# Optimization experiments

Hardware: AMD Instinct MI355X
Metric: run time of the kernel (lower is better)

Reference implementation:

```python
import jax, jax.numpy as jnp
import numpy as np

B, C, CI, HM, HC = 4, 64, 32, 128, 64  # batch, in_channels, inter_channels, main HW, cross HW
BN_EPS = 1e-5


def conv1x1(x, w, b):
    # x: [B,Cin,H,W], w: [Cout,Cin], b: [Cout]
    return jnp.einsum('bchw,oc->bohw', x, w) + b[None, :, None, None]


def _lin_coords(n_in, n_out):
    # PyTorch bilinear, align_corners=False: src = (i+0.5)*scale - 0.5, clamped
    scale = n_in / n_out
    src = (jnp.arange(n_out, dtype=jnp.float32) + 0.5) * scale - 0.5
    src = jnp.clip(src, 0.0, n_in - 1)
    i0 = jnp.floor(src).astype(jnp.int32)
    i1 = jnp.minimum(i0 + 1, n_in - 1)
    w = src - i0.astype(jnp.float32)
    return i0, i1, w


def resize_bilinear(x, h_out, w_out):
    # x: [B,C,H,W] -> [B,C,h_out,w_out], matches torch F.interpolate(mode='bilinear', align_corners=False)
    _, _, h_in, w_in = x.shape
    i0, i1, wh = _lin_coords(h_in, h_out)
    x = x[:, :, i0, :] * (1.0 - wh)[None, None, :, None] + x[:, :, i1, :] * wh[None, None, :, None]
    j0, j1, ww = _lin_coords(w_in, w_out)
    x = x[:, :, :, j0] * (1.0 - ww)[None, None, None, :] + x[:, :, :, j1] * ww[None, None, None, :]
    return x


def setup_inputs() -> dict:
    key = jax.random.key(0)
    ks = jax.random.split(key, 12)
    p = lambda k, shape, s=0.05: jax.random.normal(k, shape, dtype=jnp.float32) * s
    return {
        'main_feature': jax.random.normal(ks[0], (B, C, HM, HM), dtype=jnp.float32),
        'cross_feature': jax.random.normal(ks[1], (B, C, HC, HC), dtype=jnp.float32),
        'g_w': p(ks[2], (CI, C)), 'g_b': p(ks[3], (CI,)),
        'theta_w': p(ks[4], (CI, C)), 'theta_b': p(ks[5], (CI,)),
        'phi_w': p(ks[6], (CI, C)), 'phi_b': p(ks[7], (CI,)),
        'w_w': p(ks[8], (C, CI)), 'w_b': p(ks[9], (C,)),
        'bn_gamma': 1.0 + p(ks[10], (C,)), 'bn_beta': p(ks[11], (C,)),
    }


def reference(main_feature, cross_feature, g_w, g_b, theta_w, theta_b,
              phi_w, phi_b, w_w, w_b, bn_gamma, bn_beta):
    b, _, hc, wc = cross_feature.shape
    hm = main_feature.shape[2]
    # g(cross) -> [B, Nc, Ci]
    x = conv1x1(cross_feature, g_w, g_b).reshape(b, CI, -1).transpose(0, 2, 1)
    # theta(cross) -> [B, Ci, Nc]
    y = conv1x1(cross_feature, theta_w, theta_b).reshape(b, CI, -1)
    # phi(resize(main -> cross size)) -> [B, Nc, Ci]
    z = resize_bilinear(main_feature, hc, hc)
    z = conv1x1(z, phi_w, phi_b).reshape(b, CI, -1).transpose(0, 2, 1)
    # unscaled attention: [B, Nc, Nc]
    f = jnp.einsum('bnc,bcm->bnm', x, y)
    attn = jax.nn.softmax(f, axis=-1)
    out = jnp.einsum('bnm,bmc->bnc', attn, z)           # [B, Nc, Ci]
    out = out.transpose(0, 2, 1).reshape(b, CI, hc, wc)  # [B, Ci, Hc, Wc]
    # W: 1x1 conv + BatchNorm2d (training mode: batch statistics, biased var)
    out = conv1x1(out, w_w, w_b)
    mean = out.mean(axis=(0, 2, 3), keepdims=True)
    var = out.var(axis=(0, 2, 3), keepdims=True)
    out = (out - mean) * jax.lax.rsqrt(var + BN_EPS)
    out = out * bn_gamma[None, :, None, None] + bn_beta[None, :, None, None]
    out = resize_bilinear(out, hm, hm)
    return out + main_feature
```

## Files before the change

### kernel.cpp

```cpp
#include <hip/hip_runtime.h>
#include <hip/hip_bf16.h>


typedef __attribute__((ext_vector_type(8))) short bf16x8;
typedef __attribute__((ext_vector_type(4))) float f32x4;

#define LOG2E 1.4426950408889634f

static __device__ __forceinline__ unsigned short f2bf_bits(float x) {
    __hip_bfloat16 h = __float2bfloat16(x);
    return *(unsigned short*)&h;
}
static __device__ __forceinline__ unsigned int pk2bf(float a, float b) {
    __hip_bfloat162 h = __float22bfloat162_rn(make_float2(a, b));
    return *(unsigned int*)&h;
}

__global__ __launch_bounds__(256) void qkv_kernel(
    const float* __restrict__ cross, const float* __restrict__ mainf,
    const float* __restrict__ g_w,  const float* __restrict__ g_b,
    const float* __restrict__ th_w, const float* __restrict__ th_b,
    const float* __restrict__ ph_w, const float* __restrict__ ph_b,
    __hip_bfloat16* __restrict__ Qb, __hip_bfloat16* __restrict__ Kb,
    __hip_bfloat16* __restrict__ Vt)
{
    __shared__ float xs[64][256];
    const int kind = blockIdx.x >> 6;
    const int pblk = blockIdx.x & 63;
    const int b = pblk >> 4, n0 = (pblk & 15) << 8;
    const int t = threadIdx.x;

    const float* w  = (kind == 0) ? g_w : (kind == 1) ? th_w : ph_w;
    const float* bs = (kind == 0) ? g_b : (kind == 1) ? th_b : ph_b;

    if (kind < 2) {
        const float* src = cross + (((size_t)(b * 64)) << 12) + n0;
        const int jr = (t & 63) << 2, c0 = t >> 6;
#pragma unroll
        for (int it = 0; it < 16; ++it) {
            int c = (it << 2) | c0;
            *(float4*)&xs[c][jr] = *(const float4*)(src + ((size_t)c << 12) + jr);
        }
    } else {
        const int n = n0 + t;
        const int i2 = (n >> 6) << 1, j2 = (n & 63) << 1;
        const float* src = mainf + (((size_t)(b * 64)) << 14) + i2 * 128 + j2;
#pragma unroll 4
        for (int c = 0; c < 64; ++c) {
            const float2 a = *(const float2*)(src + ((size_t)c << 14));
            const float2 d = *(const float2*)(src + ((size_t)c << 14) + 128);
            xs[c][t] = 0.25f * ((a.x + a.y) + (d.x + d.y));
        }
    }
    __syncthreads();

    float acc[32];
#pragma unroll
    for (int ci = 0; ci < 32; ++ci) acc[ci] = bs[ci];
#pragma unroll 4
    for (int c = 0; c < 64; ++c) {
        float x = xs[c][t];
#pragma unroll
        for (int ci = 0; ci < 32; ++ci)
            acc[ci] = fmaf(w[(ci << 6) + c], x, acc[ci]);
    }

    const int pix = (b << 12) + n0 + t;
    if (kind < 2) {
        if (kind == 0) {
#pragma unroll
            for (int ci = 0; ci < 32; ++ci) acc[ci] *= LOG2E;
        }
        unsigned int u[16];
#pragma unroll
        for (int i = 0; i < 16; ++i)
            u[i] = (unsigned int)f2bf_bits(acc[2 * i]) |
                   ((unsigned int)f2bf_bits(acc[2 * i + 1]) << 16);
        __hip_bfloat16* dst = ((kind == 0) ? Qb : Kb) + (size_t)pix * 32;
        uint4* d4 = (uint4*)dst;
#pragma unroll
        for (int r = 0; r < 4; ++r)
            d4[r] = make_uint4(u[4*r], u[4*r+1], u[4*r+2], u[4*r+3]);
    } else {
        const int n = n0 + t;
#pragma unroll
        for (int ci = 0; ci < 32; ++ci)
            Vt[((size_t)((b << 5) | ci) << 12) + n] = __float2bfloat16(acc[ci]);
    }
}

__global__ __launch_bounds__(256) void attn_mfma(
    const __hip_bfloat16* __restrict__ Qb, const __hip_bfloat16* __restrict__ Kb,
    const __hip_bfloat16* __restrict__ Vt, const float* __restrict__ w_w,
    const float* __restrict__ w_b, float* __restrict__ out2)
{
    __shared__ __align__(16) __hip_bfloat16 pbuf[4][2][16][40];
    __shared__ __align__(16) float redbuf[2][64][12];
    __shared__ __align__(16) float obuf[32][36];
    const int tid = threadIdx.x, lane = tid & 63, w = tid >> 6;
    const int lo = lane & 15, c = lane >> 4;
    const int kh = w & 1, qg = w >> 1;
    const int b = blockIdx.y;
    const int qbase = (blockIdx.x << 5) + (qg << 4);

    const bf16x8 aq = *(const bf16x8*)(Qb + (((size_t)(b << 12) + qbase + lo) << 5) + (c << 3));
    const __hip_bfloat16* Kbb = Kb + ((size_t)(b << 12) << 5);
    const __hip_bfloat16* Vbb = Vt + ((size_t)(b << 5) << 12);

    f32x4 acc0 = {0.f,0.f,0.f,0.f}, acc1 = {0.f,0.f,0.f,0.f};
    float den = 0.f;
    const f32x4 z = {0.f,0.f,0.f,0.f};
    const int kq = kh << 11;
#define LDK(k)      (*(const bf16x8*)(Kbb + ((size_t)((k) + lo) << 5) + (c << 3)))
#define LDV(k, cio) (*(const bf16x8*)(Vbb + ((size_t)(lo + (cio)) << 12) + (k) + (c << 3)))

    bf16x8 k0c = LDK(kq),      k1c = LDK(kq + 16);
    bf16x8 vB0 = LDV(kq, 0),   vB1 = LDV(kq, 16);
    bf16x8 k0n = LDK(kq + 32), k1n = LDK(kq + 48);
    bf16x8 vN0 = LDV(kq + 32, 0), vN1 = LDV(kq + 32, 16);
    bf16x8 ap;

    {
        f32x4 s0 = __builtin_amdgcn_mfma_f32_16x16x32_bf16(k0c, aq, z, 0, 0, 0);
        f32x4 s1 = __builtin_amdgcn_mfma_f32_16x16x32_bf16(k1c, aq, z, 0, 0, 0);
        float p0 = __builtin_amdgcn_exp2f(s0[0]), p1 = __builtin_amdgcn_exp2f(s0[1]);
        float p2 = __builtin_amdgcn_exp2f(s0[2]), p3 = __builtin_amdgcn_exp2f(s0[3]);
        float q0 = __builtin_amdgcn_exp2f(s1[0]), q1 = __builtin_amdgcn_exp2f(s1[1]);
        float q2 = __builtin_amdgcn_exp2f(s1[2]), q3 = __builtin_amdgcn_exp2f(s1[3]);
        den += ((p0 + p1) + (p2 + p3)) + ((q0 + q1) + (q2 + q3));
        uint2 wv0 = make_uint2(pk2bf(p0, p1), pk2bf(p2, p3));
        uint2 wv1 = make_uint2(pk2bf(q0, q1), pk2bf(q2, q3));
        *(uint2*)&pbuf[w][0][lo][c << 2]        = wv0;
        *(uint2*)&pbuf[w][0][lo][16 + (c << 2)] = wv1;
        ap = *(const bf16x8*)&pbuf[w][0][lo][c << 3];
    }

#pragma unroll 2
    for (int ch = 1; ch < 64; ++ch) {
        const int kn = kq + ((ch + 1) & 63) * 32;
        bf16x8 vA0 = vB0, vA1 = vB1;
        vB0 = vN0; vB1 = vN1;
        k0c = k0n; k1c = k1n;
        k0n = LDK(kn); k1n = LDK(kn + 16);
        vN0 = LDV(kn, 0); vN1 = LDV(kn, 16);

        f32x4 s0 = __builtin_amdgcn_mfma_f32_16x16x32_bf16(k0c, aq, z, 0, 0, 0);
        f32x4 s1 = __builtin_amdgcn_mfma_f32_16x16x32_bf16(k1c, aq, z, 0, 0, 0);
        float p0 = __builtin_amdgcn_exp2f(s0[0]), p1 = __builtin_amdgcn_exp2f(s0[1]);
        float p2 = __builtin_amdgcn_exp2f(s0[2]), p3 = __builtin_amdgcn_exp2f(s0[3]);
        float q0 = __builtin_amdgcn_exp2f(s1[0]), q1 = __builtin_amdgcn_exp2f(s1[1]);
        float q2 = __builtin_amdgcn_exp2f(s1[2]), q3 = __builtin_amdgcn_exp2f(s1[3]);
        den += ((p0 + p1) + (p2 + p3)) + ((q0 + q1) + (q2 + q3));
        uint2 wv0 = make_uint2(pk2bf(p0, p1), pk2bf(p2, p3));
        uint2 wv1 = make_uint2(pk2bf(q0, q1), pk2bf(q2, q3));
        *(uint2*)&pbuf[w][ch & 1][lo][c << 2]        = wv0;
        *(uint2*)&pbuf[w][ch & 1][lo][16 + (c << 2)] = wv1;

        acc0 = __builtin_amdgcn_mfma_f32_16x16x32_bf16(ap, vA0, acc0, 0, 0, 0);
        acc1 = __builtin_amdgcn_mfma_f32_16x16x32_bf16(ap, vA1, acc1, 0, 0, 0);

        ap = *(const bf16x8*)&pbuf[w][ch & 1][lo][c << 3];
    }
    acc0 = __builtin_amdgcn_mfma_f32_16x16x32_bf16(ap, vB0, acc0, 0, 0, 0);
    acc1 = __builtin_amdgcn_mfma_f32_16x16x32_bf16(ap, vB1, acc1, 0, 0, 0);
#undef LDK
#undef LDV

    den += __shfl_xor(den, 16);
    den += __shfl_xor(den, 32);

    if (kh) {
        f32x4* rb = (f32x4*)&redbuf[qg][lane][0];
        rb[0] = acc0; rb[1] = acc1;
        f32x4 dv = {den, 0.f, 0.f, 0.f};
        rb[2] = dv;
    }
    __syncthreads();
    if (kh == 0) {
        const f32x4* rb = (const f32x4*)&redbuf[qg][lane][0];
        f32x4 a0 = rb[0], a1 = rb[1], dv = rb[2];
        acc0 += a0; acc1 += a1;
        den += dv[0];
#pragma unroll
        for (int r = 0; r < 4; ++r) {
            float inv = 1.0f / __shfl(den, (c << 2) | r);
            obuf[(qg << 4) | (c << 2) | r][lo]      = acc0[r] * inv;
            obuf[(qg << 4) | (c << 2) | r][16 + lo] = acc1[r] * inv;
        }
    }
    __syncthreads();

    const int q = tid & 31, cog = tid >> 5;
    float ov[32];
    const float4* orow = (const float4*)&obuf[q][0];
#pragma unroll
    for (int k4 = 0; k4 < 8; ++k4) {
        float4 t = orow[k4];
        ov[4*k4] = t.x; ov[4*k4+1] = t.y; ov[4*k4+2] = t.z; ov[4*k4+3] = t.w;
    }
    float* dstbase = out2 + (((size_t)(b << 6)) << 12) + (blockIdx.x << 5) + q;
#pragma unroll
    for (int kk = 0; kk < 8; ++kk) {
        int co = (kk << 3) | cog;
        const float4* wr = (const float4*)&w_w[co << 5];
        float acc = w_b[co];
#pragma unroll
        for (int k4 = 0; k4 < 8; ++k4) {
            float4 t = wr[k4];
            acc = fmaf(t.x, ov[4*k4],   acc);
            acc = fmaf(t.y, ov[4*k4+1], acc);
            acc = fmaf(t.z, ov[4*k4+2], acc);
            acc = fmaf(t.w, ov[4*k4+3], acc);
        }
        dstbase[(size_t)co << 12] = acc;
    }
}

__global__ __launch_bounds__(256) void stats_kernel(
    const float* __restrict__ out2, float* __restrict__ stats1)
{
    int co = blockIdx.x >> 2, b = blockIdx.x & 3, t = threadIdx.x;
    const float* p = out2 + ((size_t)((b << 6) | co) << 12);
    float s = 0.f, s2 = 0.f;
#pragma unroll
    for (int ii = 0; ii < 16; ++ii) {
        float v = p[(ii << 8) | t];
        s += v; s2 = fmaf(v, v, s2);
    }
    __shared__ float rs[256], rs2[256];
    rs[t] = s; rs2[t] = s2;
    __syncthreads();
    for (int off = 128; off > 0; off >>= 1) {
        if (t < off) { rs[t] += rs[t + off]; rs2[t] += rs2[t + off]; }
        __syncthreads();
    }
    if (t == 0) {
        stats1[blockIdx.x * 2]     = rs[0];
        stats1[blockIdx.x * 2 + 1] = rs2[0];
    }
}

__global__ __launch_bounds__(256) void up_kernel(
    const float* __restrict__ out2, const float* __restrict__ stats1,
    const float* __restrict__ gamma, const float* __restrict__ beta,
    const float* __restrict__ mainf, float* __restrict__ out)
{
    int gid = blockIdx.x * 256 + threadIdx.x;
    int j4 = (gid & 31) << 2;
    int i  = (gid >> 5) & 127;
    int co = (gid >> 12) & 63;
    int b  = gid >> 18;

    float sm = 0.f, sq = 0.f;
#pragma unroll
    for (int bb = 0; bb < 4; ++bb) {
        sm += stats1[((co << 2) | bb) * 2];
        sq += stats1[((co << 2) | bb) * 2 + 1];
    }
    float mean = sm * (1.0f / 16384.0f);
    float var  = sq * (1.0f / 16384.0f) - mean * mean;
    float inv  = rsqrtf(var + 1e-5f);
    float scale = gamma[co] * inv;
    float shift = beta[co] - mean * scale;

    int ih = i >> 1;
    int k0, k1; float wi;
    if (i & 1)       { k0 = ih;     k1 = (ih < 63) ? ih + 1 : 63; wi = 0.25f; }
    else if (ih == 0){ k0 = 0;      k1 = 0;                       wi = 0.0f;  }
    else             { k0 = ih - 1; k1 = ih;                      wi = 0.75f; }

    const float* p0r = out2 + ((size_t)((b << 6) | co) << 12) + (k0 << 6);
    const float* p1r = out2 + ((size_t)((b << 6) | co) << 12) + (k1 << 6);

    float res[4];
#pragma unroll
    for (int jj = 0; jj < 4; ++jj) {
        int j = j4 | jj;
        int il = j >> 1;
        int l0, l1; float wj;
        if (j & 1)       { l0 = il;     l1 = (il < 63) ? il + 1 : 63; wj = 0.25f; }
        else if (il == 0){ l0 = 0;      l1 = 0;                       wj = 0.0f;  }
        else             { l0 = il - 1; l1 = il;                      wj = 0.75f; }
        float v00 = p0r[l0], v01 = p0r[l1];
        float v10 = p1r[l0], v11 = p1r[l1];
        float top = v00 + wj * (v01 - v00);
        float bot = v10 + wj * (v11 - v10);
        float v = top + wi * (bot - top);
        res[jj] = fmaf(v, scale, shift);
    }
    size_t idx = (((size_t)((b << 6) | co)) << 14) + (i << 7) + j4;
    float4 m4 = *(const float4*)(mainf + idx);
    *(float4*)(out + idx) = make_float4(res[0] + m4.x, res[1] + m4.y,
                                        res[2] + m4.z, res[3] + m4.w);
}

extern "C" void kernel_launch(void* const* d_in, const int* in_sizes, int n_in,
                              void* d_out, int out_size, void* d_ws, size_t ws_size,
                              hipStream_t stream)
{
    const float* mainf = (const float*)d_in[0];
    const float* cross = (const float*)d_in[1];
    const float* g_w   = (const float*)d_in[2];
    const float* g_b   = (const float*)d_in[3];
    const float* th_w  = (const float*)d_in[4];
    const float* th_b  = (const float*)d_in[5];
    const float* ph_w  = (const float*)d_in[6];
    const float* ph_b  = (const float*)d_in[7];
    const float* w_w   = (const float*)d_in[8];
    const float* w_b   = (const float*)d_in[9];
    const float* gamma = (const float*)d_in[10];
    const float* beta  = (const float*)d_in[11];
    float* out = (float*)d_out;

    __hip_bfloat16* Qb = (__hip_bfloat16*)d_ws;
    __hip_bfloat16* Kb = Qb + 524288;
    __hip_bfloat16* Vt = Kb + 524288;
    float* out2   = (float*)(Vt + 524288);
    float* stats1 = out2 + 1048576;

    qkv_kernel<<<192, 256, 0, stream>>>(cross, mainf, g_w, g_b, th_w, th_b,
                                        ph_w, ph_b, Qb, Kb, Vt);
    attn_mfma<<<dim3(128, 4), 256, 0, stream>>>(Qb, Kb, Vt, w_w, w_b, out2);
    stats_kernel<<<256, 256, 0, stream>>>(out2, stats1);
    up_kernel<<<4096, 256, 0, stream>>>(out2, stats1, gamma, beta, mainf, out);
}
```

Before: 170.5 us.

## Fuse all stages into one persistent kernel with grid barriers

Merges the QKV projection, attention, BN statistics and upsample kernels into a single 512-block kernel separated by two software grid barriers. BN statistics are now accumulated with atomics in the attention epilogue, which removes the separate stats pass. The QKV stage is re-split into 384 smaller blocks so it spreads over more CUs. This removes per-launch overhead and one full read of out2. It relies on all 512 blocks being co-resident, which launch_bounds(256,2) is meant to ensure, and adds an init kernel plus barrier spin cost.

```diff
diff --git a/kernel.cpp b/kernel.cpp
--- a/kernel.cpp
+++ b/kernel.cpp
@@ -16,282 +16,303 @@
     return *(unsigned int*)&h;
 }
 
-__global__ __launch_bounds__(256) void qkv_kernel(
-    const float* __restrict__ cross, const float* __restrict__ mainf,
+union __align__(16) Smem {
+    float xs[64][128];
+    struct {
+        __hip_bfloat16 pbuf[4][2][16][40];
+        float redbuf[2][64][12];
+        float obuf[32][36];
+    } at;
+};
+
+__global__ __launch_bounds__(256) void init_kernel(float* stats, unsigned* bar) {
+    if (threadIdx.x < 128) stats[threadIdx.x] = 0.f;
+    if (threadIdx.x < 2)   bar[threadIdx.x] = 0u;
+}
+
+static __device__ __forceinline__ void grid_barrier(unsigned* bar, int idx) {
+    __threadfence();
+    __syncthreads();
+    if (threadIdx.x == 0) {
+        atomicAdd(&bar[idx], 1u);
+        while (__hip_atomic_load(&bar[idx], __ATOMIC_RELAXED,
+                                 __HIP_MEMORY_SCOPE_AGENT) < 512u) {
+            __builtin_amdgcn_s_sleep(2);
+        }
+    }
+    __syncthreads();
+    __threadfence();
+}
+
+__global__ __launch_bounds__(256, 2) void mega_kernel(
+    const float* __restrict__ mainf, const float* __restrict__ cross,
     const float* __restrict__ g_w,  const float* __restrict__ g_b,
     const float* __restrict__ th_w, const float* __restrict__ th_b,
     const float* __restrict__ ph_w, const float* __restrict__ ph_b,
+    const float* __restrict__ w_w,  const float* __restrict__ w_b,
+    const float* __restrict__ gamma, const float* __restrict__ beta,
     __hip_bfloat16* __restrict__ Qb, __hip_bfloat16* __restrict__ Kb,
-    __hip_bfloat16* __restrict__ Vt)
+    __hip_bfloat16* __restrict__ Vt, float* __restrict__ out2,
+    float* __restrict__ stats, unsigned* __restrict__ bar,
+    float* __restrict__ out)
 {
-    __shared__ float xs[64][256];
-    const int kind = blockIdx.x >> 6;
-    const int pblk = blockIdx.x & 63;
-    const int b = pblk >> 4, n0 = (pblk & 15) << 8;
-    const int t = threadIdx.x;
-
-    const float* w  = (kind == 0) ? g_w : (kind == 1) ? th_w : ph_w;
-    const float* bs = (kind == 0) ? g_b : (kind == 1) ? th_b : ph_b;
-
-    if (kind < 2) {
-        const float* src = cross + (((size_t)(b * 64)) << 12) + n0;
-        const int jr = (t & 63) << 2, c0 = t >> 6;
-#pragma unroll
-        for (int it = 0; it < 16; ++it) {
-            int c = (it << 2) | c0;
-            *(float4*)&xs[c][jr] = *(const float4*)(src + ((size_t)c << 12) + jr);
-        }
-    } else {
-        const int n = n0 + t;
-        const int i2 = (n >> 6) << 1, j2 = (n & 63) << 1;
-        const float* src = mainf + (((size_t)(b * 64)) << 14) + i2 * 128 + j2;
+    __shared__ Smem smem;
+    const int tid = threadIdx.x;
+
+    {
+        const int kb = blockIdx.x;
+        if (kb < 384) {
+            const int kind = kb >> 7;
+            const int sub  = kb & 127;
+            const int b    = sub >> 5;
+            const int n0   = (sub & 31) << 7;
+            const float* w  = (kind == 0) ? g_w : (kind == 1) ? th_w : ph_w;
+            const float* bs = (kind == 0) ? g_b : (kind == 1) ? th_b : ph_b;
+
+            if (kind < 2) {
+                const float* src = cross + (((size_t)(b * 64)) << 12) + n0;
+                const int jr = (tid & 31) << 2, c0 = tid >> 5;
+#pragma unroll
+                for (int it = 0; it < 8; ++it) {
+                    int c = (it << 3) | c0;
+                    *(float4*)&smem.xs[c][jr] = *(const float4*)(src + ((size_t)c << 12) + jr);
+                }
+            } else {
+                const int px = tid & 127, chh = tid >> 7;
+                const int n = n0 + px;
+                const int i2 = (n >> 6) << 1, j2 = (n & 63) << 1;
+                const float* src = mainf + (((size_t)(b * 64)) << 14) + i2 * 128 + j2;
 #pragma unroll 4
-        for (int c = 0; c < 64; ++c) {
-            const float2 a = *(const float2*)(src + ((size_t)c << 14));
-            const float2 d = *(const float2*)(src + ((size_t)c << 14) + 128);
-            xs[c][t] = 0.25f * ((a.x + a.y) + (d.x + d.y));
+                for (int cc = 0; cc < 32; ++cc) {
+                    int c = (chh << 5) | cc;
+                    const float2 a = *(const float2*)(src + ((size_t)c << 14));
+                    const float2 d = *(const float2*)(src + ((size_t)c << 14) + 128);
+                    smem.xs[c][px] = 0.25f * ((a.x + a.y) + (d.x + d.y));
+                }
+            }
+            __syncthreads();
+
+            const int px = tid & 127, cih = tid >> 7, ci0 = cih << 4;
+            float acc[16];
+#pragma unroll
+            for (int j = 0; j < 16; ++j) acc[j] = bs[ci0 + j];
+#pragma unroll 4
+            for (int c = 0; c < 64; ++c) {
+                float x = smem.xs[c][px];
+#pragma unroll
+                for (int j = 0; j < 16; ++j)
+                    acc[j] = fmaf(w[((ci0 + j) << 6) + c], x, acc[j]);
+            }
+            const int n = n0 + px;
+            const int pix = (b << 12) + n;
+            if (kind < 2) {
+                if (kind == 0) {
+#pragma unroll
+                    for (int j = 0; j < 16; ++j) acc[j] *= LOG2E;
+                }
+                unsigned int u[8];
+#pragma unroll
+                for (int i = 0; i < 8; ++i)
+                    u[i] = (unsigned int)f2bf_bits(acc[2 * i]) |
+                           ((unsigned int)f2bf_bits(acc[2 * i + 1]) << 16);
+                uint4* d4 = (uint4*)(((kind == 0) ? Qb : Kb) + (size_t)pix * 32 + ci0);
+                d4[0] = make_uint4(u[0], u[1], u[2], u[3]);
+                d4[1] = make_uint4(u[4], u[5], u[6], u[7]);
+            } else {
+#pragma unroll
+                for (int j = 0; j < 16; ++j)
+                    Vt[((size_t)((b << 5) | (ci0 + j)) << 12) + n] = __float2bfloat16(acc[j]);
+            }
         }
     }
-    __syncthreads();
-
-    float acc[32];
-#pragma unroll
-    for (int ci = 0; ci < 32; ++ci) acc[ci] = bs[ci];
-#pragma unroll 4
-    for (int c = 0; c < 64; ++c) {
-        float x = xs[c][t];
-#pragma unroll
-        for (int ci = 0; ci < 32; ++ci)
-            acc[ci] = fmaf(w[(ci << 6) + c], x, acc[ci]);
-    }
-
-    const int pix = (b << 12) + n0 + t;
-    if (kind < 2) {
-        if (kind == 0) {
-#pragma unroll
-            for (int ci = 0; ci < 32; ++ci) acc[ci] *= LOG2E;
-        }
-        unsigned int u[16];
-#pragma unroll
-        for (int i = 0; i < 16; ++i)
-            u[i] = (unsigned int)f2bf_bits(acc[2 * i]) |
-                   ((unsigned int)f2bf_bits(acc[2 * i + 1]) << 16);
-        __hip_bfloat16* dst = ((kind == 0) ? Qb : Kb) + (size_t)pix * 32;
-        uint4* d4 = (uint4*)dst;
-#pragma unroll
-        for (int r = 0; r < 4; ++r)
-            d4[r] = make_uint4(u[4*r], u[4*r+1], u[4*r+2], u[4*r+3]);
-    } else {
-        const int n = n0 + t;
-#pragma unroll
-        for (int ci = 0; ci < 32; ++ci)
-            Vt[((size_t)((b << 5) | ci) << 12) + n] = __float2bfloat16(acc[ci]);
-    }
-}
-
-__global__ __launch_bounds__(256) void attn_mfma(
-    const __hip_bfloat16* __restrict__ Qb, const __hip_bfloat16* __restrict__ Kb,
-    const __hip_bfloat16* __restrict__ Vt, const float* __restrict__ w_w,
-    const float* __restrict__ w_b, float* __restrict__ out2)
-{
-    __shared__ __align__(16) __hip_bfloat16 pbuf[4][2][16][40];
-    __shared__ __align__(16) float redbuf[2][64][12];
-    __shared__ __align__(16) float obuf[32][36];
-    const int tid = threadIdx.x, lane = tid & 63, w = tid >> 6;
-    const int lo = lane & 15, c = lane >> 4;
-    const int kh = w & 1, qg = w >> 1;
-    const int b = blockIdx.y;
-    const int qbase = (blockIdx.x << 5) + (qg << 4);
-
-    const bf16x8 aq = *(const bf16x8*)(Qb + (((size_t)(b << 12) + qbase + lo) << 5) + (c << 3));
-    const __hip_bfloat16* Kbb = Kb + ((size_t)(b << 12) << 5);
-    const __hip_bfloat16* Vbb = Vt + ((size_t)(b << 5) << 12);
-
-    f32x4 acc0 = {0.f,0.f,0.f,0.f}, acc1 = {0.f,0.f,0.f,0.f};
-    float den = 0.f;
-    const f32x4 z = {0.f,0.f,0.f,0.f};
-    const int kq = kh << 11;
+    grid_barrier(bar, 0);
+
+    {
+        const int lane = tid & 63, w = tid >> 6;
+        const int lo = lane & 15, c = lane >> 4;
+        const int kh = w & 1, qg = w >> 1;
+        const int b = blockIdx.x >> 7, bx = blockIdx.x & 127;
+        const int qbase = (bx << 5) + (qg << 4);
+
+        const bf16x8 aq = *(const bf16x8*)(Qb + (((size_t)(b << 12) + qbase + lo) << 5) + (c << 3));
+        const __hip_bfloat16* Kbb = Kb + ((size_t)(b << 12) << 5);
+        const __hip_bfloat16* Vbb = Vt + ((size_t)(b << 5) << 12);
+
+        f32x4 acc0 = {0.f,0.f,0.f,0.f}, acc1 = {0.f,0.f,0.f,0.f};
+        float den = 0.f;
+        const f32x4 z = {0.f,0.f,0.f,0.f};
+        const int kq = kh << 11;
 #define LDK(k)      (*(const bf16x8*)(Kbb + ((size_t)((k) + lo) << 5) + (c << 3)))
 #define LDV(k, cio) (*(const bf16x8*)(Vbb + ((size_t)(lo + (cio)) << 12) + (k) + (c << 3)))
 
-    bf16x8 k0c = LDK(kq),      k1c = LDK(kq + 16);
-    bf16x8 vB0 = LDV(kq, 0),   vB1 = LDV(kq, 16);
-    bf16x8 k0n = LDK(kq + 32), k1n = LDK(kq + 48);
-    bf16x8 vN0 = LDV(kq + 32, 0), vN1 = LDV(kq + 32, 16);
-    bf16x8 ap;
-
-    {
-        f32x4 s0 = __builtin_amdgcn_mfma_f32_16x16x32_bf16(k0c, aq, z, 0, 0, 0);
-        f32x4 s1 = __builtin_amdgcn_mfma_f32_16x16x32_bf16(k1c, aq, z, 0, 0, 0);
-        float p0 = __builtin_amdgcn_exp2f(s0[0]), p1 = __builtin_amdgcn_exp2f(s0[1]);
-        float p2 = __builtin_amdgcn_exp2f(s0[2]), p3 = __builtin_amdgcn_exp2f(s0[3]);
-        float q0 = __builtin_amdgcn_exp2f(s1[0]), q1 = __builtin_amdgcn_exp2f(s1[1]);
-        float q2 = __builtin_amdgcn_exp2f(s1[2]), q3 = __builtin_amdgcn_exp2f(s1[3]);
-        den += ((p0 + p1) + (p2 + p3)) + ((q0 + q1) + (q2 + q3));
-        uint2 wv0 = make_uint2(pk2bf(p0, p1), pk2bf(p2, p3));
-        uint2 wv1 = make_uint2(pk2bf(q0, q1), pk2bf(q2, q3));
-        *(uint2*)&pbuf[w][0][lo][c << 2]        = wv0;
-        *(uint2*)&pbuf[w][0][lo][16 + (c << 2)] = wv1;
-        ap = *(const bf16x8*)&pbuf[w][0][lo][c << 3];
-    }
+        bf16x8 k0c = LDK(kq),      k1c = LDK(kq + 16);
+        bf16x8 vB0 = LDV(kq, 0),   vB1 = LDV(kq, 16);
+        bf16x8 k0n = LDK(kq + 32), k1n = LDK(kq + 48);
+        bf16x8 vN0 = LDV(kq + 32, 0), vN1 = LDV(kq + 32, 16);
+        bf16x8 ap;
+
+        {
+            f32x4 s0 = __builtin_amdgcn_mfma_f32_16x16x32_bf16(k0c, aq, z, 0, 0, 0);
+            f32x4 s1 = __builtin_amdgcn_mfma_f32_16x16x32_bf16(k1c, aq, z, 0, 0, 0);
+            float p0 = __builtin_amdgcn_exp2f(s0[0]), p1 = __builtin_amdgcn_exp2f(s0[1]);
+            float p2 = __builtin_amdgcn_exp2f(s0[2]), p3 = __builtin_amdgcn_exp2f(s0[3]);
+            float q0 = __builtin_amdgcn_exp2f(s1[0]), q1 = __builtin_amdgcn_exp2f(s1[1]);
+            float q2 = __builtin_amdgcn_exp2f(s1[2]), q3 = __builtin_amdgcn_exp2f(s1[3]);
+            den += ((p0 + p1) + (p2 + p3)) + ((q0 + q1) + (q2 + q3));
+            uint2 wv0 = make_uint2(pk2bf(p0, p1), pk2bf(p2, p3));
+            uint2 wv1 = make_uint2(pk2bf(q0, q1), pk2bf(q2, q3));
+            *(uint2*)&smem.at.pbuf[w][0][lo][c << 2]        = wv0;
+            *(uint2*)&smem.at.pbuf[w][0][lo][16 + (c << 2)] = wv1;
+            ap = *(const bf16x8*)&smem.at.pbuf[w][0][lo][c << 3];
+        }
 
 #pragma unroll 2
-    for (int ch = 1; ch < 64; ++ch) {
-        const int kn = kq + ((ch + 1) & 63) * 32;
-        bf16x8 vA0 = vB0, vA1 = vB1;
-        vB0 = vN0; vB1 = vN1;
-        k0c = k0n; k1c = k1n;
-        k0n = LDK(kn); k1n = LDK(kn + 16);
-        vN0 = LDV(kn, 0); vN1 = LDV(kn, 16);
-
-        f32x4 s0 = __builtin_amdgcn_mfma_f32_16x16x32_bf16(k0c, aq, z, 0, 0, 0);
-        f32x4 s1 = __builtin_amdgcn_mfma_f32_16x16x32_bf16(k1c, aq, z, 0, 0, 0);
-        float p0 = __builtin_amdgcn_exp2f(s0[0]), p1 = __builtin_amdgcn_exp2f(s0[1]);
-        float p2 = __builtin_amdgcn_exp2f(s0[2]), p3 = __builtin_amdgcn_exp2f(s0[3]);
-        float q0 = __builtin_amdgcn_exp2f(s1[0]), q1 = __builtin_amdgcn_exp2f(s1[1]);
-        float q2 = __builtin_amdgcn_exp2f(s1[2]), q3 = __builtin_amdgcn_exp2f(s1[3]);
-        den += ((p0 + p1) + (p2 + p3)) + ((q0 + q1) + (q2 + q3));
-        uint2 wv0 = make_uint2(pk2bf(p0, p1), pk2bf(p2, p3));
-        uint2 wv1 = make_uint2(pk2bf(q0, q1), pk2bf(q2, q3));
-        *(uint2*)&pbuf[w][ch & 1][lo][c << 2]        = wv0;
-        *(uint2*)&pbuf[w][ch & 1][lo][16 + (c << 2)] = wv1;
-
-        acc0 = __builtin_amdgcn_mfma_f32_16x16x32_bf16(ap, vA0, acc0, 0, 0, 0);
-        acc1 = __builtin_amdgcn_mfma_f32_16x16x32_bf16(ap, vA1, acc1, 0, 0, 0);
-
-        ap = *(const bf16x8*)&pbuf[w][ch & 1][lo][c << 3];
-    }
-    acc0 = __builtin_amdgcn_mfma_f32_16x16x32_bf16(ap, vB0, acc0, 0, 0, 0);
-    acc1 = __builtin_amdgcn_mfma_f32_16x16x32_bf16(ap, vB1, acc1, 0, 0, 0);
+        for (int ch = 1; ch < 64; ++ch) {
+            const int kn = kq + ((ch + 1) & 63) * 32;
+            bf16x8 vA0 = vB0, vA1 = vB1;
+            vB0 = vN0; vB1 = vN1;
+            k0c = k0n; k1c = k1n;
+            k0n = LDK(kn); k1n = LDK(kn + 16);
+            vN0 = LDV(kn, 0); vN1 = LDV(kn, 16);
+
+            f32x4 s0 = __builtin_amdgcn_mfma_f32_16x16x32_bf16(k0c, aq, z, 0, 0, 0);
+            f32x4 s1 = __builtin_amdgcn_mfma_f32_16x16x32_bf16(k1c, aq, z, 0, 0, 0);
+            float p0 = __builtin_amdgcn_exp2f(s0[0]), p1 = __builtin_amdgcn_exp2f(s0[1]);
+            float p2 = __builtin_amdgcn_exp2f(s0[2]), p3 = __builtin_amdgcn_exp2f(s0[3]);
+            float q0 = __builtin_amdgcn_exp2f(s1[0]), q1 = __builtin_amdgcn_exp2f(s1[1]);
+            float q2 = __builtin_amdgcn_exp2f(s1[2]), q3 = __builtin_amdgcn_exp2f(s1[3]);
+            den += ((p0 + p1) + (p2 + p3)) + ((q0 + q1) + (q2 + q3));
+            uint2 wv0 = make_uint2(pk2bf(p0, p1), pk2bf(p2, p3));
+            uint2 wv1 = make_uint2(pk2bf(q0, q1), pk2bf(q2, q3));
+            *(uint2*)&smem.at.pbuf[w][ch & 1][lo][c << 2]        = wv0;
+            *(uint2*)&smem.at.pbuf[w][ch & 1][lo][16 + (c << 2)] = wv1;
+
+            acc0 = __builtin_amdgcn_mfma_f32_16x16x32_bf16(ap, vA0, acc0, 0, 0, 0);
+            acc1 = __builtin_amdgcn_mfma_f32_16x16x32_bf16(ap, vA1, acc1, 0, 0, 0);
+
+            ap = *(const bf16x8*)&smem.at.pbuf[w][ch & 1][lo][c << 3];
+        }
+        acc0 = __builtin_amdgcn_mfma_f32_16x16x32_bf16(ap, vB0, acc0, 0, 0, 0);
+        acc1 = __builtin_amdgcn_mfma_f32_16x16x32_bf16(ap, vB1, acc1, 0, 0, 0);
 #undef LDK
 #undef LDV
 
-    den += __shfl_xor(den, 16);
-    den += __shfl_xor(den, 32);
-
-    if (kh) {
-        f32x4* rb = (f32x4*)&redbuf[qg][lane][0];
-        rb[0] = acc0; rb[1] = acc1;
-        f32x4 dv = {den, 0.f, 0.f, 0.f};
-        rb[2] = dv;
+        den += __shfl_xor(den, 16);
+        den += __shfl_xor(den, 32);
+
+        if (kh) {
+            f32x4* rb = (f32x4*)&smem.at.redbuf[qg][lane][0];
+            rb[0] = acc0; rb[1] = acc1;
+            f32x4 dv = {den, 0.f, 0.f, 0.f};
+            rb[2] = dv;
+        }
+        __syncthreads();
+        if (kh == 0) {
+            const f32x4* rb = (const f32x4*)&smem.at.redbuf[qg][lane][0];
+            f32x4 a0 = rb[0], a1 = rb[1], dv = rb[2];
+            acc0 += a0; acc1 += a1;
+            den += dv[0];
+#pragma unroll
+            for (int r = 0; r < 4; ++r) {
+                float inv = 1.0f / __shfl(den, (c << 2) | r);
+                smem.at.obuf[(qg << 4) | (c << 2) | r][lo]      = acc0[r] * inv;
+                smem.at.obuf[(qg << 4) | (c << 2) | r][16 + lo] = acc1[r] * inv;
+            }
+        }
+        __syncthreads();
+
+        const int q = tid & 31, cog = tid >> 5;
+        float ov[32];
+        const float4* orow = (const float4*)&smem.at.obuf[q][0];
+#pragma unroll
+        for (int k4 = 0; k4 < 8; ++k4) {
+            float4 t = orow[k4];
+            ov[4*k4] = t.x; ov[4*k4+1] = t.y; ov[4*k4+2] = t.z; ov[4*k4+3] = t.w;
+        }
+        float* dstbase = out2 + (((size_t)(b << 6)) << 12) + (bx << 5) + q;
+        float vs[8], vs2[8];
+#pragma unroll
+        for (int kk = 0; kk < 8; ++kk) {
+            int co = (kk << 3) | cog;
+            const float4* wr = (const float4*)&w_w[co << 5];
+            float acc = w_b[co];
+#pragma unroll
+            for (int k4 = 0; k4 < 8; ++k4) {
+                float4 t = wr[k4];
+                acc = fmaf(t.x, ov[4*k4],   acc);
+                acc = fmaf(t.y, ov[4*k4+1], acc);
+                acc = fmaf(t.z, ov[4*k4+2], acc);
+                acc = fmaf(t.w, ov[4*k4+3], acc);
+            }
+            dstbase[(size_t)co << 12] = acc;
+            vs[kk] = acc; vs2[kk] = acc * acc;
+        }
+#pragma unroll
+        for (int off = 1; off < 32; off <<= 1) {
+#pragma unroll
+            for (int kk = 0; kk < 8; ++kk) {
+                vs[kk]  += __shfl_xor(vs[kk],  off);
+                vs2[kk] += __shfl_xor(vs2[kk], off);
+            }
+        }
+        if ((lane & 31) == 0) {
+#pragma unroll
+            for (int kk = 0; kk < 8; ++kk) {
+                int co = (kk << 3) | cog;
+                atomicAdd(&stats[co],      vs[kk]);
+                atomicAdd(&stats[64 + co], vs2[kk]);
+            }
+        }
     }
-    __syncthreads();
-    if (kh == 0) {
-        const f32x4* rb = (const f32x4*)&redbuf[qg][lane][0];
-        f32x4 a0 = rb[0], a1 = rb[1], dv = rb[2];
-        acc0 += a0; acc1 += a1;
-        den += dv[0];
-#pragma unroll
-        for (int r = 0; r < 4; ++r) {
-            float inv = 1.0f / __shfl(den, (c << 2) | r);
-            obuf[(qg << 4) | (c << 2) | r][lo]      = acc0[r] * inv;
-            obuf[(qg << 4) | (c << 2) | r][16 + lo] = acc1[r] * inv;
+    grid_barrier(bar, 1);
+
+    {
+        const int flat = blockIdx.x * 256 + tid;
+#pragma unroll 2
+        for (int u = 0; u < 8; ++u) {
+            const int gid = flat + (u << 17);
+            const int j4 = (gid & 31) << 2;
+            const int i  = (gid >> 5) & 127;
+            const int co = (gid >> 12) & 63;
+            const int b  = gid >> 18;
+
+            float mean = stats[co] * (1.0f / 16384.0f);
+            float var  = stats[64 + co] * (1.0f / 16384.0f) - mean * mean;
+            float inv  = rsqrtf(var + 1e-5f);
+            float scale = gamma[co] * inv;
+            float shift = beta[co] - mean * scale;
+
+            int ih = i >> 1;
+            int k0, k1; float wi;
+            if (i & 1)       { k0 = ih;     k1 = (ih < 63) ? ih + 1 : 63; wi = 0.25f; }
+            else if (ih == 0){ k0 = 0;      k1 = 0;                       wi = 0.0f;  }
+            else             { k0 = ih - 1; k1 = ih;                      wi = 0.75f; }
+
+            const float* p0r = out2 + ((size_t)((b << 6) | co) << 12) + (k0 << 6);
+            const float* p1r = out2 + ((size_t)((b << 6) | co) << 12) + (k1 << 6);
+
+            float res[4];
+#pragma unroll
+            for (int jj = 0; jj < 4; ++jj) {
+                int j = j4 | jj;
+                int il = j >> 1;
+                int l0, l1; float wj;
+                if (j & 1)       { l0 = il;     l1 = (il < 63) ? il + 1 : 63; wj = 0.25f; }
+                else if (il == 0){ l0 = 0;      l1 = 0;                       wj = 0.0f;  }
+                else             { l0 = il - 1; l1 = il;                      wj = 0.75f; }
+                float v00 = p0r[l0], v01 = p0r[l1];
+                float v10 = p1r[l0], v11 = p1r[l1];
+                float top = v00 + wj * (v01 - v00);
+                float bot = v10 + wj * (v11 - v10);
+                float v = top + wi * (bot - top);
+                res[jj] = fmaf(v, scale, shift);
+            }
+            size_t idx = (((size_t)((b << 6) | co)) << 14) + (i << 7) + j4;
+            float4 m4 = *(const float4*)(mainf + idx);
+            *(float4*)(out + idx) = make_float4(res[0] + m4.x, res[1] + m4.y,
+                                                res[2] + m4.z, res[3] + m4.w);
         }
     }
-    __syncthreads();
-
-    const int q = tid & 31, cog = tid >> 5;
-    float ov[32];
-    const float4* orow = (const float4*)&obuf[q][0];
-#pragma unroll
-    for (int k4 = 0; k4 < 8; ++k4) {
-        float4 t = orow[k4];
-        ov[4*k4] = t.x; ov[4*k4+1] = t.y; ov[4*k4+2] = t.z; ov[4*k4+3] = t.w;
-    }
-    float* dstbase = out2 + (((size_t)(b << 6)) << 12) + (blockIdx.x << 5) + q;
-#pragma unroll
-    for (int kk = 0; kk < 8; ++kk) {
-        int co = (kk << 3) | cog;
-        const float4* wr = (const float4*)&w_w[co << 5];
-        float acc = w_b[co];
-#pragma unroll
-        for (int k4 = 0; k4 < 8; ++k4) {
-            float4 t = wr[k4];
-            acc = fmaf(t.x, ov[4*k4],   acc);
-            acc = fmaf(t.y, ov[4*k4+1], acc);
-            acc = fmaf(t.z, ov[4*k4+2], acc);
-            acc = fmaf(t.w, ov[4*k4+3], acc);
-        }
-        dstbase[(size_t)co << 12] = acc;
-    }
-}
-
-__global__ __launch_bounds__(256) void stats_kernel(
-    const float* __restrict__ out2, float* __restrict__ stats1)
-{
-    int co = blockIdx.x >> 2, b = blockIdx.x & 3, t = threadIdx.x;
-    const float* p = out2 + ((size_t)((b << 6) | co) << 12);
-    float s = 0.f, s2 = 0.f;
-#pragma unroll
-    for (int ii = 0; ii < 16; ++ii) {
-        float v = p[(ii << 8) | t];
-        s += v; s2 = fmaf(v, v, s2);
-    }
-    __shared__ float rs[256], rs2[256];
-    rs[t] = s; rs2[t] = s2;
-    __syncthreads();
-    for (int off = 128; off > 0; off >>= 1) {
-        if (t < off) { rs[t] += rs[t + off]; rs2[t] += rs2[t + off]; }
-        __syncthreads();
-    }
-    if (t == 0) {
-        stats1[blockIdx.x * 2]     = rs[0];
-        stats1[blockIdx.x * 2 + 1] = rs2[0];
-    }
-}
-
-__global__ __launch_bounds__(256) void up_kernel(
-    const float* __restrict__ out2, const float* __restrict__ stats1,
-    const float* __restrict__ gamma, const float* __restrict__ beta,
-    const float* __restrict__ mainf, float* __restrict__ out)
-{
-    int gid = blockIdx.x * 256 + threadIdx.x;
-    int j4 = (gid & 31) << 2;
-    int i  = (gid >> 5) & 127;
-    int co = (gid >> 12) & 63;
-    int b  = gid >> 18;
-
-    float sm = 0.f, sq = 0.f;
-#pragma unroll
-    for (int bb = 0; bb < 4; ++bb) {
-        sm += stats1[((co << 2) | bb) * 2];
-        sq += stats1[((co << 2) | bb) * 2 + 1];
-    }
-    float mean = sm * (1.0f / 16384.0f);
-    float var  = sq * (1.0f / 16384.0f) - mean * mean;
-    float inv  = rsqrtf(var + 1e-5f);
-    float scale = gamma[co] * inv;
-    float shift = beta[co] - mean * scale;
-
-    int ih = i >> 1;
-    int k0, k1; float wi;
-    if (i & 1)       { k0 = ih;     k1 = (ih < 63) ? ih + 1 : 63; wi = 0.25f; }
-    else if (ih == 0){ k0 = 0;      k1 = 0;                       wi = 0.0f;  }
-    else             { k0 = ih - 1; k1 = ih;                      wi = 0.75f; }
-
-    const float* p0r = out2 + ((size_t)((b << 6) | co) << 12) + (k0 << 6);
-    const float* p1r = out2 + ((size_t)((b << 6) | co) << 12) + (k1 << 6);
-
-    float res[4];
-#pragma unroll
-    for (int jj = 0; jj < 4; ++jj) {
-        int j = j4 | jj;
-        int il = j >> 1;
-        int l0, l1; float wj;
-        if (j & 1)       { l0 = il;     l1 = (il < 63) ? il + 1 : 63; wj = 0.25f; }
-        else if (il == 0){ l0 = 0;      l1 = 0;                       wj = 0.0f;  }
-        else             { l0 = il - 1; l1 = il;                      wj = 0.75f; }
-        float v00 = p0r[l0], v01 = p0r[l1];
-        float v10 = p1r[l0], v11 = p1r[l1];
-        float top = v00 + wj * (v01 - v00);
-        float bot = v10 + wj * (v11 - v10);
-        float v = top + wi * (bot - top);
-        res[jj] = fmaf(v, scale, shift);
-    }
-    size_t idx = (((size_t)((b << 6) | co)) << 14) + (i << 7) + j4;
-    float4 m4 = *(const float4*)(mainf + idx);
-    *(float4*)(out + idx) = make_float4(res[0] + m4.x, res[1] + m4.y,
-                                        res[2] + m4.z, res[3] + m4.w);
 }
 
 extern "C" void kernel_launch(void* const* d_in, const int* in_sizes, int n_in,
@@ -315,12 +336,12 @@
     __hip_bfloat16* Qb = (__hip_bfloat16*)d_ws;
     __hip_bfloat16* Kb = Qb + 524288;
     __hip_bfloat16* Vt = Kb + 524288;
-    float* out2   = (float*)(Vt + 524288);
-    float* stats1 = out2 + 1048576;
-
-    qkv_kernel<<<192, 256, 0, stream>>>(cross, mainf, g_w, g_b, th_w, th_b,
-                                        ph_w, ph_b, Qb, Kb, Vt);
-    attn_mfma<<<dim3(128, 4), 256, 0, stream>>>(Qb, Kb, Vt, w_w, w_b, out2);
-    stats_kernel<<<256, 256, 0, stream>>>(out2, stats1);
-    up_kernel<<<4096, 256, 0, stream>>>(out2, stats1, gamma, beta, mainf, out);
-}
+    float* out2  = (float*)(Vt + 524288);
+    float* stats = out2 + 1048576;
+    unsigned* bar = (unsigned*)(stats + 128);
+
+    init_kernel<<<1, 256, 0, stream>>>(stats, bar);
+    mega_kernel<<<512, 256, 0, stream>>>(mainf, cross, g_w, g_b, th_w, th_b,
+                                         ph_w, ph_b, w_w, w_b, gamma, beta,
+                                         Qb, Kb, Vt, out2, stats, bar, out);
+}
```

New measurement: 419.2 us. 2.46x slower.

## Split attention keys across four waves and halve QKV block work

Applied to the files above, without the earlier changes.

In the attention kernel, each block now handles 16 queries, and its four waves each cover a quarter of the keys, with a three-way shared-memory reduction at the end. This doubles the grid to 1024 blocks so more of the GPU's compute units are busy. The QKV projection kernel now uses 128 pixels per block, and each thread computes 16 of the 32 output channels, doubling that grid as well. The cost is that every Q tile is reloaded by twice as many blocks, the reduction has more steps, and the epilogue convolution reads the weights more often.

```diff
diff --git a/kernel.cpp b/kernel.cpp
--- a/kernel.cpp
+++ b/kernel.cpp
@@ -24,68 +24,68 @@
     __hip_bfloat16* __restrict__ Qb, __hip_bfloat16* __restrict__ Kb,
     __hip_bfloat16* __restrict__ Vt)
 {
-    __shared__ float xs[64][256];
-    const int kind = blockIdx.x >> 6;
-    const int pblk = blockIdx.x & 63;
-    const int b = pblk >> 4, n0 = (pblk & 15) << 8;
-    const int t = threadIdx.x;
-
+    __shared__ float xs[64][128];
+    const int kind = blockIdx.x >> 7;
+    const int sub  = blockIdx.x & 127;
+    const int b    = sub >> 5;
+    const int n0   = (sub & 31) << 7;
+    const int tid  = threadIdx.x;
     const float* w  = (kind == 0) ? g_w : (kind == 1) ? th_w : ph_w;
     const float* bs = (kind == 0) ? g_b : (kind == 1) ? th_b : ph_b;
 
     if (kind < 2) {
         const float* src = cross + (((size_t)(b * 64)) << 12) + n0;
-        const int jr = (t & 63) << 2, c0 = t >> 6;
-#pragma unroll
-        for (int it = 0; it < 16; ++it) {
-            int c = (it << 2) | c0;
+        const int jr = (tid & 31) << 2, c0 = tid >> 5;
+#pragma unroll
+        for (int it = 0; it < 8; ++it) {
+            int c = (it << 3) | c0;
             *(float4*)&xs[c][jr] = *(const float4*)(src + ((size_t)c << 12) + jr);
         }
     } else {
-        const int n = n0 + t;
+        const int px = tid & 127, chh = tid >> 7;
+        const int n = n0 + px;
         const int i2 = (n >> 6) << 1, j2 = (n & 63) << 1;
         const float* src = mainf + (((size_t)(b * 64)) << 14) + i2 * 128 + j2;
 #pragma unroll 4
-        for (int c = 0; c < 64; ++c) {
+        for (int cc = 0; cc < 32; ++cc) {
+            int c = (chh << 5) | cc;
             const float2 a = *(const float2*)(src + ((size_t)c << 14));
             const float2 d = *(const float2*)(src + ((size_t)c << 14) + 128);
-            xs[c][t] = 0.25f * ((a.x + a.y) + (d.x + d.y));
+            xs[c][px] = 0.25f * ((a.x + a.y) + (d.x + d.y));
         }
     }
     __syncthreads();
 
-    float acc[32];
-#pragma unroll
-    for (int ci = 0; ci < 32; ++ci) acc[ci] = bs[ci];
+    const int px = tid & 127, cih = tid >> 7, ci0 = cih << 4;
+    float acc[16];
+#pragma unroll
+    for (int j = 0; j < 16; ++j) acc[j] = bs[ci0 + j];
 #pragma unroll 4
     for (int c = 0; c < 64; ++c) {
-        float x = xs[c][t];
-#pragma unroll
-        for (int ci = 0; ci < 32; ++ci)
-            acc[ci] = fmaf(w[(ci << 6) + c], x, acc[ci]);
-    }
-
-    const int pix = (b << 12) + n0 + t;
+        float x = xs[c][px];
+#pragma unroll
+        for (int j = 0; j < 16; ++j)
+            acc[j] = fmaf(w[((ci0 + j) << 6) + c], x, acc[j]);
+    }
+    const int n = n0 + px;
+    const int pix = (b << 12) + n;
     if (kind < 2) {
         if (kind == 0) {
 #pragma unroll
-            for (int ci = 0; ci < 32; ++ci) acc[ci] *= LOG2E;
-        }
-        unsigned int u[16];
-#pragma unroll
-        for (int i = 0; i < 16; ++i)
+            for (int j = 0; j < 16; ++j) acc[j] *= LOG2E;
+        }
+        unsigned int u[8];
+#pragma unroll
+        for (int i = 0; i < 8; ++i)
             u[i] = (unsigned int)f2bf_bits(acc[2 * i]) |
                    ((unsigned int)f2bf_bits(acc[2 * i + 1]) << 16);
-        __hip_bfloat16* dst = ((kind == 0) ? Qb : Kb) + (size_t)pix * 32;
-        uint4* d4 = (uint4*)dst;
-#pragma unroll
-        for (int r = 0; r < 4; ++r)
-            d4[r] = make_uint4(u[4*r], u[4*r+1], u[4*r+2], u[4*r+3]);
+        uint4* d4 = (uint4*)(((kind == 0) ? Qb : Kb) + (size_t)pix * 32 + ci0);
+        d4[0] = make_uint4(u[0], u[1], u[2], u[3]);
+        d4[1] = make_uint4(u[4], u[5], u[6], u[7]);
     } else {
-        const int n = n0 + t;
-#pragma unroll
-        for (int ci = 0; ci < 32; ++ci)
-            Vt[((size_t)((b << 5) | ci) << 12) + n] = __float2bfloat16(acc[ci]);
+#pragma unroll
+        for (int j = 0; j < 16; ++j)
+            Vt[((size_t)((b << 5) | (ci0 + j)) << 12) + n] = __float2bfloat16(acc[j]);
     }
 }
 
@@ -95,13 +95,11 @@
     const float* __restrict__ w_b, float* __restrict__ out2)
 {
     __shared__ __align__(16) __hip_bfloat16 pbuf[4][2][16][40];
-    __shared__ __align__(16) float redbuf[2][64][12];
-    __shared__ __align__(16) float obuf[32][36];
+    __shared__ __align__(16) float redbuf[3][64][12];
+    __shared__ __align__(16) float obuf[16][36];
     const int tid = threadIdx.x, lane = tid & 63, w = tid >> 6;
     const int lo = lane & 15, c = lane >> 4;
-    const int kh = w & 1, qg = w >> 1;
-    const int b = blockIdx.y;
-    const int qbase = (blockIdx.x << 5) + (qg << 4);
+    const int b = blockIdx.y, qbase = blockIdx.x << 4;
 
     const bf16x8 aq = *(const bf16x8*)(Qb + (((size_t)(b << 12) + qbase + lo) << 5) + (c << 3));
     const __hip_bfloat16* Kbb = Kb + ((size_t)(b << 12) << 5);
@@ -110,7 +108,7 @@
     f32x4 acc0 = {0.f,0.f,0.f,0.f}, acc1 = {0.f,0.f,0.f,0.f};
     float den = 0.f;
     const f32x4 z = {0.f,0.f,0.f,0.f};
-    const int kq = kh << 11;
+    const int kq = w << 10;
 #define LDK(k)      (*(const bf16x8*)(Kbb + ((size_t)((k) + lo) << 5) + (c << 3)))
 #define LDV(k, cio) (*(const bf16x8*)(Vbb + ((size_t)(lo + (cio)) << 12) + (k) + (c << 3)))
 
@@ -136,8 +134,8 @@
     }
 
 #pragma unroll 2
-    for (int ch = 1; ch < 64; ++ch) {
-        const int kn = kq + ((ch + 1) & 63) * 32;
+    for (int ch = 1; ch < 32; ++ch) {
+        const int kn = kq + ((ch + 1) & 31) * 32;
         bf16x8 vA0 = vB0, vA1 = vB1;
         vB0 = vN0; vB1 = vN1;
         k0c = k0n; k1c = k1n;
@@ -169,28 +167,31 @@
     den += __shfl_xor(den, 16);
     den += __shfl_xor(den, 32);
 
-    if (kh) {
-        f32x4* rb = (f32x4*)&redbuf[qg][lane][0];
+    if (w) {
+        f32x4* rb = (f32x4*)&redbuf[w - 1][lane][0];
         rb[0] = acc0; rb[1] = acc1;
         f32x4 dv = {den, 0.f, 0.f, 0.f};
         rb[2] = dv;
     }
     __syncthreads();
-    if (kh == 0) {
-        const f32x4* rb = (const f32x4*)&redbuf[qg][lane][0];
-        f32x4 a0 = rb[0], a1 = rb[1], dv = rb[2];
-        acc0 += a0; acc1 += a1;
-        den += dv[0];
+    if (w == 0) {
+#pragma unroll
+        for (int ww = 0; ww < 3; ++ww) {
+            const f32x4* rb = (const f32x4*)&redbuf[ww][lane][0];
+            f32x4 a0 = rb[0], a1 = rb[1], dv = rb[2];
+            acc0 += a0; acc1 += a1;
+            den += dv[0];
+        }
 #pragma unroll
         for (int r = 0; r < 4; ++r) {
             float inv = 1.0f / __shfl(den, (c << 2) | r);
-            obuf[(qg << 4) | (c << 2) | r][lo]      = acc0[r] * inv;
-            obuf[(qg << 4) | (c << 2) | r][16 + lo] = acc1[r] * inv;
+            obuf[(c << 2) | r][lo]      = acc0[r] * inv;
+            obuf[(c << 2) | r][16 + lo] = acc1[r] * inv;
         }
     }
     __syncthreads();
 
-    const int q = tid & 31, cog = tid >> 5;
+    const int q = tid & 15, cog = tid >> 4;
     float ov[32];
     const float4* orow = (const float4*)&obuf[q][0];
 #pragma unroll
@@ -198,10 +199,10 @@
         float4 t = orow[k4];
         ov[4*k4] = t.x; ov[4*k4+1] = t.y; ov[4*k4+2] = t.z; ov[4*k4+3] = t.w;
     }
-    float* dstbase = out2 + (((size_t)(b << 6)) << 12) + (blockIdx.x << 5) + q;
-#pragma unroll
-    for (int kk = 0; kk < 8; ++kk) {
-        int co = (kk << 3) | cog;
+    float* dstbase = out2 + (((size_t)(b << 6)) << 12) + qbase + q;
+#pragma unroll
+    for (int kk = 0; kk < 4; ++kk) {
+        int co = (kk << 4) | cog;
         const float4* wr = (const float4*)&w_w[co << 5];
         float acc = w_b[co];
 #pragma unroll
@@ -318,9 +319,9 @@
     float* out2   = (float*)(Vt + 524288);
     float* stats1 = out2 + 1048576;
 
-    qkv_kernel<<<192, 256, 0, stream>>>(cross, mainf, g_w, g_b, th_w, th_b,
+    qkv_kernel<<<384, 256, 0, stream>>>(cross, mainf, g_w, g_b, th_w, th_b,
                                         ph_w, ph_b, Qb, Kb, Vt);
-    attn_mfma<<<dim3(128, 4), 256, 0, stream>>>(Qb, Kb, Vt, w_w, w_b, out2);
+    attn_mfma<<<dim3(256, 4), 256, 0, stream>>>(Qb, Kb, Vt, w_w, w_b, out2);
     stats_kernel<<<256, 256, 0, stream>>>(out2, stats1);
     up_kernel<<<4096, 256, 0, stream>>>(out2, stats1, gamma, beta, mainf, out);
 }
```

New measurement: 168.0 us. No clear change (-1.5%).
